# Performance work log

Hardware: AMD Instinct MI355X
Metric: run time of the kernel (lower is better)

## Reference

```python
import jax, jax.numpy as jnp
import numpy as np

B, N, F_RAW = 4, 131072, 9
GX, GY = 512, 512
EMB = 16
D_IN = F_RAW + EMB  # 25
D_OUT = 64
MAX_PT = 64
EPS = 1e-5


def _bn(x, g, b, w):
    # masked batch-statistics BatchNorm1d (training-mode forward); w: [P] 0/1 mask
    wc = w[:, None]
    cnt = jnp.maximum(w.sum(), 1.0)
    mu = (x * wc).sum(0) / cnt
    var = (((x - mu) ** 2) * wc).sum(0) / cnt
    return (x - mu) * jax.lax.rsqrt(var + EPS) * g + b


def setup_inputs() -> dict:
    key = jax.random.key(0)
    ks = jax.random.split(key, 12)
    pt_fea = jax.random.normal(ks[0], (B, N, F_RAW), jnp.float32)
    xy_ind = jax.random.randint(ks[1], (B, N, 2), 0, GX)
    pt_label = jax.random.randint(ks[2], (B, N, 1), 0, 32)

    def lin_w(k, i, o):
        return (jax.random.normal(k, (i, o), jnp.float32) / np.float32(np.sqrt(i)))

    return {
        "pt_fea": pt_fea, "xy_ind": xy_ind, "pt_label": pt_label,
        "emb": jax.random.normal(ks[3], (32, EMB), jnp.float32),
        "bn0_g": jnp.ones((D_IN,), jnp.float32), "bn0_b": jnp.zeros((D_IN,), jnp.float32),
        "w1": lin_w(ks[4], D_IN, 32), "b1": jnp.zeros((32,), jnp.float32),
        "bn1_g": jnp.ones((32,), jnp.float32), "bn1_b": jnp.zeros((32,), jnp.float32),
        "w2": lin_w(ks[5], 32, 64), "b2": jnp.zeros((64,), jnp.float32),
        "bn2_g": jnp.ones((64,), jnp.float32), "bn2_b": jnp.zeros((64,), jnp.float32),
        "w3": lin_w(ks[6], 64, D_OUT), "b3": jnp.zeros((D_OUT,), jnp.float32),
    }


def reference(pt_fea, xy_ind, pt_label, emb, bn0_g, bn0_b, w1, b1, bn1_g, bn1_b,
              w2, b2, bn2_g, bn2_b, w3, b3):
    P = B * N
    fea = pt_fea.reshape(P, F_RAW)
    ind = xy_ind.reshape(P, 2)
    batch_idx = jnp.repeat(jnp.arange(P // N), N)
    vox = (batch_idx * GX + ind[:, 0]) * GY + ind[:, 1]  # linearized (b, x, y)
    S = B * GX * GY

    # rank of each point within its voxel group (identity permutation; no shuffle)
    order = jnp.argsort(vox)  # stable
    sv = vox[order]
    pos = jnp.arange(P)
    is_new = jnp.concatenate([jnp.ones((1,), bool), sv[1:] != sv[:-1]])
    start = jax.lax.cummax(jnp.where(is_new, pos, 0))
    rank = jnp.zeros((P,), jnp.int32).at[order].set((pos - start).astype(jnp.int32))
    remain = rank < MAX_PT  # keep at most MAX_PT points per voxel
    mask = remain.astype(fea.dtype)

    x = jnp.concatenate([fea, emb[pt_label.reshape(P)]], axis=-1)  # [P, 25]
    x = _bn(x, bn0_g, bn0_b, mask)
    x = jax.nn.relu(_bn(x @ w1 + b1, bn1_g, bn1_b, mask))
    x = jax.nn.relu(_bn(x @ w2 + b2, bn2_g, bn2_b, mask))
    x = x @ w3 + b3  # [P, 64]

    # scatter_max over voxel groups; dropped points go to dummy segment S
    seg = jnp.where(remain, vox, S)
    pooled = jax.ops.segment_max(x, seg, num_segments=S + 1)[:S]
    cnt = jax.ops.segment_sum(mask, seg, num_segments=S + 1)[:S]
    pooled = jnp.where(cnt[:, None] > 0, pooled, 0.0)  # empty voxels stay 0

    bev = pooled.reshape(B, GX, GY, D_OUT).transpose(0, 3, 1, 2)  # [B, C, GX, GY]
    out = jax.lax.reduce_window(bev, -jnp.inf, jax.lax.max,
                                (1, 1, 3, 3), (1, 1, 1, 1),
                                [(0, 0), (0, 0), (1, 1), (1, 1)])
    return out
```

## Files before the change

### kernel.cpp

```cpp
#include <hip/hip_runtime.h>
#include <hip/hip_bf16.h>
#include <math.h>

typedef unsigned int u32;
typedef unsigned short u16;
typedef __attribute__((ext_vector_type(8))) short bf8v;
typedef __attribute__((ext_vector_type(4))) float f4v;

#define B_    4
#define N_    131072
#define P_    (B_*N_)
#define GX_   512
#define GY_   512
#define S_    (B_*GX_*GY_)
#define D_IN  25
#define MAXPT 64
#define EPS_  1e-5f
#define REP_  32

__device__ __forceinline__ float bf2f(u16 h){ return __uint_as_float(((u32)h)<<16); }
__device__ __forceinline__ u16 f2bf(float f){ u32 b=__float_as_uint(f); u32 r=b+0x7FFFu+((b>>16)&1u); return (u16)(r>>16); }

__device__ __forceinline__ void unpack8(uint4 a, float* x){
  x[0]=bf2f((u16)(a.x&0xFFFFu)); x[1]=bf2f((u16)(a.x>>16));
  x[2]=bf2f((u16)(a.y&0xFFFFu)); x[3]=bf2f((u16)(a.y>>16));
  x[4]=bf2f((u16)(a.z&0xFFFFu)); x[5]=bf2f((u16)(a.z>>16));
  x[6]=bf2f((u16)(a.w&0xFFFFu)); x[7]=bf2f((u16)(a.w>>16));
}

__device__ __forceinline__ void buildFeat(int p, const float* __restrict__ fea,
    const int* __restrict__ lab, const float* __restrict__ emb, float* v)
{
  #pragma unroll
  for (int k=0;k<9;k++) v[k] = fea[p*9+k];
  int l = lab[p];
  const float4* er = (const float4*)(emb + l*16);
  float4 e0=er[0], e1=er[1], e2=er[2], e3=er[3];
  v[9]=e0.x; v[10]=e0.y; v[11]=e0.z; v[12]=e0.w;
  v[13]=e1.x; v[14]=e1.y; v[15]=e1.z; v[16]=e1.w;
  v[17]=e2.x; v[18]=e2.y; v[19]=e2.z; v[20]=e2.w;
  v[21]=e3.x; v[22]=e3.y; v[23]=e3.z; v[24]=e3.w;
  #pragma unroll
  for (int k=25;k<32;k++) v[k]=0.f;
}

__device__ __forceinline__ void stats32(float* tile, float* sS, float* sQ,
                                        const float v[32], int tid)
{
  #pragma unroll
  for (int k=0;k<32;k++) tile[tid*33+k] = v[k];
  __syncthreads();
  int c = tid & 31, g = tid >> 5;
  float s=0.f, q=0.f;
  #pragma unroll
  for (int r=0;r<32;r++){
    float x = tile[(g*32+r)*33 + c];
    s += x; q = fmaf(x,x,q);
  }
  atomicAdd(&sS[c], s); atomicAdd(&sQ[c], q);
  __syncthreads();
}

__global__ __launch_bounds__(256) void zeroK(u32* __restrict__ cnt, float* __restrict__ stats)
{
  int t = blockIdx.x*256 + threadIdx.x;
  ((uint4*)cnt)[t] = make_uint4(0,0,0,0);
  if (blockIdx.x == 0){
    #pragma unroll
    for (int k=0;k<8;k++)
      ((uint4*)stats)[threadIdx.x*8+k] = make_uint4(0,0,0,0);
  }
}

__global__ __launch_bounds__(256) void passA(
    const float* __restrict__ fea, const int* __restrict__ xy, const int* __restrict__ lab,
    const float* __restrict__ emb, u32* __restrict__ cnt, u32* __restrict__ voxflag,
    float* __restrict__ partA)
{
  __shared__ float tile[256*33];
  __shared__ float sS[32], sQ[32];
  int tid = threadIdx.x;
  if (tid < 32){ sS[tid]=0.f; sQ[tid]=0.f; }
  int p = blockIdx.x*256 + tid;
  int b = p >> 17;
  int ix = xy[2*p], iy = xy[2*p+1];
  u32 vox = ((u32)b<<18) + ((u32)ix<<9) + (u32)iy;
  u32 rank = atomicAdd(&cnt[vox], 1u);
  bool remain = rank < MAXPT;
  voxflag[p] = vox | (min(rank,63u)<<20) | (remain ? 0x80000000u : 0u);

  float v[32];
  buildFeat(p, fea, lab, emb, v);
  if (!remain){
    #pragma unroll
    for (int k=0;k<32;k++) v[k]=0.f;
  }
  __syncthreads();
  stats32(tile, sS, sQ, v, tid);
  int rep = blockIdx.x & (REP_-1);
  if (tid < 32) atomicAdd(&partA[rep*64+tid], sS[tid]);
  else if (tid < 64) atomicAdd(&partA[rep*64+tid], sQ[tid-32]);
}

__global__ __launch_bounds__(256) void scan1(const u32* __restrict__ cnt,
                                             u32* __restrict__ scanned, u32* __restrict__ blockSum)
{
  __shared__ u32 ts[256];
  int tid = threadIdx.x;
  size_t base = (size_t)blockIdx.x*1024 + tid*4;
  uint4 c4 = *(const uint4*)(cnt + base);
  u32 c0=min(c4.x,64u), c1=min(c4.y,64u), c2=min(c4.z,64u), c3=min(c4.w,64u);
  u32 tsum = c0+c1+c2+c3;
  ts[tid]=tsum; __syncthreads();
  for (int off=1; off<256; off<<=1){
    u32 v = (tid>=off)? ts[tid-off] : 0u; __syncthreads();
    ts[tid]+=v; __syncthreads();
  }
  u32 ex = ts[tid]-tsum;
  uint4 o; o.x=ex; o.y=ex+c0; o.z=ex+c0+c1; o.w=ex+c0+c1+c2;
  *(uint4*)(scanned+base)=o;
  if (tid==255) blockSum[blockIdx.x]=ts[255];
}

__global__ __launch_bounds__(256) void scan2p0(u32* __restrict__ bs, u32* __restrict__ cntW,
    const float* __restrict__ partA,
    const float* __restrict__ g0, const float* __restrict__ b0,
    const float* __restrict__ w1, const float* __restrict__ b1,
    float* __restrict__ W1T, float* __restrict__ c1f)
{
  __shared__ u32 ts[256];
  __shared__ float red[64];
  __shared__ float s0[32], t0[32];
  __shared__ float Wsh;
  int tid=threadIdx.x;
  uint4 c4 = *(uint4*)(bs + tid*4);
  u32 tsum=c4.x+c4.y+c4.z+c4.w;
  ts[tid]=tsum; __syncthreads();
  for (int off=1;off<256;off<<=1){ u32 v=(tid>=off)?ts[tid-off]:0u; __syncthreads(); ts[tid]+=v; __syncthreads(); }
  u32 ex=ts[tid]-tsum;
  uint4 o; o.x=ex; o.y=ex+c4.x; o.z=ex+c4.x+c4.y; o.w=ex+c4.x+c4.y+c4.z;
  *(uint4*)(bs+tid*4)=o;
  if (tid==255){ *cntW = ts[255]; Wsh = fmaxf((float)ts[255],1.f); }
  if (tid < 64){
    float acc=0.f;
    for (int r=0;r<REP_;r++) acc += partA[r*64+tid];
    red[tid]=acc;
  }
  __syncthreads();
  if (tid < D_IN){
    float W = Wsh;
    float mu = red[tid]/W;
    float var = fmaxf(red[32+tid]/W - mu*mu, 0.f);
    float s = g0[tid]*rsqrtf(var+EPS_);
    s0[tid]=s; t0[tid]=b0[tid]-mu*s;
  }
  __syncthreads();
  if (tid < 32){
    float acc = b1[tid];
    #pragma unroll
    for (int i=0;i<D_IN;i++) acc = fmaf(t0[i], w1[i*32+tid], acc);
    c1f[tid] = acc;
    for (int i=0;i<32;i++) W1T[tid*32+i] = (i<D_IN)? s0[i]*w1[i*32+tid] : 0.f;
  }
}

__global__ void p1k(const float* __restrict__ partB, const u32* __restrict__ cntW,
                    const float* __restrict__ g, const float* __restrict__ bb,
                    float* __restrict__ sOut, float* __restrict__ tOut)
{
  int tid = threadIdx.x;
  float s=0.f, q=0.f;
  for (int r=0;r<REP_;r++){ s += partB[r*64+tid]; q += partB[r*64+32+tid]; }
  float W = fmaxf((float)(*cntW),1.f);
  float mu = s/W, var = fmaxf(q/W-mu*mu,0.f);
  float sc = g[tid]*rsqrtf(var+EPS_);
  sOut[tid]=sc; tOut[tid]=bb[tid]-mu*sc;
}
__global__ void p2k(const float* __restrict__ partC, const u32* __restrict__ cntW,
                    const float* __restrict__ g, const float* __restrict__ bb,
                    float* __restrict__ sOut, float* __restrict__ tOut)
{
  __shared__ float red[128];
  int tid = threadIdx.x;
  float acc=0.f;
  for (int r=0;r<REP_;r++) acc += partC[r*128+tid];
  red[tid]=acc;
  __syncthreads();
  if (tid < 64){
    float W = fmaxf((float)(*cntW),1.f);
    float mu = red[tid]/W, var = fmaxf(red[64+tid]/W-mu*mu,0.f);
    float s = g[tid]*rsqrtf(var+EPS_);
    sOut[tid]=s; tOut[tid]=bb[tid]-mu*s;
  }
}

__global__ __launch_bounds__(256) void passB(
    const float* __restrict__ fea, const int* __restrict__ lab, const float* __restrict__ emb,
    const u32* __restrict__ voxflag,
    const float* __restrict__ W1T, const float* __restrict__ c1f,
    u16* __restrict__ y1, float* __restrict__ partB)
{
  __shared__ float tile[256*33];
  __shared__ float sS[32], sQ[32];
  int tid = threadIdx.x;
  if (tid < 32){ sS[tid]=0.f; sQ[tid]=0.f; }
  int p = blockIdx.x*256 + tid;
  float x[32];
  buildFeat(p, fea, lab, emb, x);
  bool flag = (voxflag[p]>>31) != 0;
  float a[32];
  u32 outp[16];
  #pragma unroll
  for (int cc=0; cc<16; cc++){
    int c0 = 2*cc;
    float a0=c1f[c0], a1=c1f[c0+1];
    #pragma unroll
    for (int i=0;i<32;i++){ a0=fmaf(x[i], W1T[c0*32+i], a0); a1=fmaf(x[i], W1T[(c0+1)*32+i], a1); }
    if(!flag){a0=0.f;a1=0.f;}
    a[c0]=a0; a[c0+1]=a1;
    outp[cc] = (u32)f2bf(a0) | ((u32)f2bf(a1)<<16);
  }
  uint4* dst = (uint4*)(y1 + (size_t)p*32);
  dst[0]=make_uint4(outp[0],outp[1],outp[2],outp[3]);
  dst[1]=make_uint4(outp[4],outp[5],outp[6],outp[7]);
  dst[2]=make_uint4(outp[8],outp[9],outp[10],outp[11]);
  dst[3]=make_uint4(outp[12],outp[13],outp[14],outp[15]);
  __syncthreads();
  stats32(tile, sS, sQ, a, tid);
  int rep = blockIdx.x & (REP_-1);
  if (tid < 32) atomicAdd(&partB[rep*64+tid], sS[tid]);
  else if (tid < 64) atomicAdd(&partB[rep*64+tid], sQ[tid-32]);
}

__global__ __launch_bounds__(256) void passCM(const u16* __restrict__ y1,
    const u32* __restrict__ voxflag,
    const float* __restrict__ s1, const float* __restrict__ t1,
    const float* __restrict__ w2, const float* __restrict__ b2,
    u16* __restrict__ y2, float* __restrict__ partC)
{
  __shared__ u16 zt4[4][16*72];
  __shared__ float s1s[32], t1s[32];
  __shared__ float sS[64], sQ[64];
  int tid = threadIdx.x;
  if (tid < 32){ s1s[tid]=s1[tid]; t1s[tid]=t1[tid]; }
  if (tid < 64){ sS[tid]=0.f; sQ[tid]=0.f; }
  __syncthreads();
  int wv = tid>>6, l = tid&63;
  int p0 = blockIdx.x*64 + wv*16;
  int m = l&15, kc = l>>4;
  u16* zt = zt4[wv];

  bf8v Bf[4];
  #pragma unroll
  for (int nt=0;nt<4;nt++){
    #pragma unroll
    for (int j=0;j<8;j++)
      Bf[nt][j] = (short)f2bf(w2[(kc*8+j)*64 + nt*16 + m]);
  }
  uint4 ra = *(const uint4*)(y1 + (size_t)(p0+m)*32 + kc*8);
  float xv[8]; unpack8(ra, xv);
  bf8v Af;
  #pragma unroll
  for (int j=0;j<8;j++){
    int ch = kc*8+j;
    Af[j] = (short)f2bf(fmaxf(fmaf(xv[j], s1s[ch], t1s[ch]), 0.f));
  }
  unsigned long long msk = __ballot((l<16) && ((voxflag[p0+l]>>31)!=0));

  f4v acc[4];
  #pragma unroll
  for (int nt=0;nt<4;nt++){
    float bb = b2[nt*16+m];
    acc[nt] = (f4v){bb,bb,bb,bb};
    acc[nt] = __builtin_amdgcn_mfma_f32_16x16x32_bf16(Af, Bf[nt], acc[nt], 0,0,0);
  }
  #pragma unroll
  for (int nt=0;nt<4;nt++){
    #pragma unroll
    for (int r=0;r<4;r++){
      int row = kc*4+r;
      u16 val = ((msk>>row)&1ull) ? f2bf(acc[nt][r]) : (u16)0;
      zt[row*72 + nt*16+m] = val;
    }
  }
  __syncthreads();
  {
    float s=0.f, q=0.f;
    #pragma unroll
    for (int mi=0;mi<16;mi++){ float v = bf2f(zt[mi*72 + l]); s+=v; q=fmaf(v,v,q); }
    atomicAdd(&sS[l], s); atomicAdd(&sQ[l], q);
  }
  {
    int mm = l>>2, q4 = l&3;
    const uint4* src = (const uint4*)(zt + mm*72 + q4*16);
    uint4 v0 = src[0], v1 = src[1];
    uint4* dy = (uint4*)(y2 + (size_t)(p0+mm)*64 + q4*16);
    dy[0]=v0; dy[1]=v1;
  }
  __syncthreads();
  int rep = blockIdx.x & (REP_-1);
  if (tid < 64) atomicAdd(&partC[rep*128+tid], sS[tid]);
  else if (tid < 128) atomicAdd(&partC[rep*128+tid], sQ[tid-64]);
}

__global__ __launch_bounds__(256) void zpassM(const u16* __restrict__ y2,
    const u32* __restrict__ voxflag, const u32* __restrict__ scanned, const u32* __restrict__ bsum,
    const float* __restrict__ s2, const float* __restrict__ t2,
    const float* __restrict__ w3, const float* __restrict__ b3, u16* __restrict__ z)
{
  __shared__ u16 zt4[4][16*72];
  __shared__ float s2s[64], t2s[64];
  int tid = threadIdx.x;
  if (tid < 64){ s2s[tid]=s2[tid]; t2s[tid]=t2[tid]; }
  __syncthreads();
  int wv = tid>>6, l = tid&63;
  int p0 = blockIdx.x*64 + wv*16;
  int m = l&15, kc = l>>4;
  u16* zt = zt4[wv];

  bf8v Bf[4][2];
  #pragma unroll
  for (int nt=0;nt<4;nt++){
    #pragma unroll
    for (int kt=0;kt<2;kt++){
      #pragma unroll
      for (int j=0;j<8;j++)
        Bf[nt][kt][j] = (short)f2bf(w3[(kc*8+j+32*kt)*64 + nt*16 + m]);
    }
  }
  uint4 r0 = *(const uint4*)(y2 + (size_t)(p0+m)*64 + kc*8);
  uint4 r1 = *(const uint4*)(y2 + (size_t)(p0+m)*64 + 32 + kc*8);
  float x0[8], x1[8]; unpack8(r0,x0); unpack8(r1,x1);
  bf8v A0, A1;
  #pragma unroll
  for (int j=0;j<8;j++){
    int c0 = kc*8+j, c1 = 32+kc*8+j;
    A0[j] = (short)f2bf(fmaxf(fmaf(x0[j], s2s[c0], t2s[c0]), 0.f));
    A1[j] = (short)f2bf(fmaxf(fmaf(x1[j], s2s[c1], t2s[c1]), 0.f));
  }
  f4v acc[4];
  #pragma unroll
  for (int nt=0;nt<4;nt++){
    float bb = b3[nt*16+m];
    acc[nt] = (f4v){bb,bb,bb,bb};
    acc[nt] = __builtin_amdgcn_mfma_f32_16x16x32_bf16(A0, Bf[nt][0], acc[nt], 0,0,0);
    acc[nt] = __builtin_amdgcn_mfma_f32_16x16x32_bf16(A1, Bf[nt][1], acc[nt], 0,0,0);
  }
  #pragma unroll
  for (int nt=0;nt<4;nt++){
    #pragma unroll
    for (int r=0;r<4;r++)
      zt[(kc*4+r)*72 + nt*16+m] = f2bf(acc[nt][r]);
  }
  __syncthreads();
  int mm = l>>2, q4 = l&3;
  u32 vf = voxflag[p0+mm];
  if (vf>>31){
    u32 vox = vf & 0xFFFFFu;
    u32 rank = (vf>>20)&63u;
    u32 slot = scanned[vox] + bsum[vox>>10] + rank;
    const uint4* src = (const uint4*)(zt + mm*72 + q4*16);
    uint4 v0 = src[0], v1 = src[1];
    uint4* dz = (uint4*)(z + (size_t)slot*64 + q4*16);
    dz[0]=v0; dz[1]=v1;
  }
}

__global__ __launch_bounds__(256) void poolT(
    const u32* __restrict__ scanned, const u32* __restrict__ bsum, const u32* __restrict__ cnt,
    const u16* __restrict__ z, u16* __restrict__ pooledT)
{
  __shared__ u16 lds[32][66];
  int tid = threadIdx.x;
  int g = tid>>3, sub = tid&7;
  int v = blockIdx.x*32 + g;
  u32 n = min(cnt[v],64u);
  u16 r[8];
  if (n==0){
    #pragma unroll
    for (int j=0;j<8;j++) r[j]=0;
  } else {
    u32 st = scanned[v] + bsum[v>>10];
    float m[8];
    #pragma unroll
    for (int j=0;j<8;j++) m[j] = -__builtin_inff();
    for (u32 k=0;k<n;k++){
      uint4 a = *(const uint4*)(z + (size_t)(st+k)*64 + sub*8);
      float x[8]; unpack8(a,x);
      #pragma unroll
      for (int j=0;j<8;j++) m[j]=fmaxf(m[j],x[j]);
    }
    #pragma unroll
    for (int j=0;j<8;j++) r[j]=f2bf(m[j]);
  }
  #pragma unroll
  for (int j=0;j<8;j++) lds[g][sub*8+j] = r[j];
  __syncthreads();
  int c = tid>>2, q = tid&3;
  int v0 = blockIdx.x*32;
  int iy0 = v0 & 511, ix = (v0>>9)&511, b = v0>>18;
  u16 o[8];
  #pragma unroll
  for (int m2=0;m2<8;m2++) o[m2] = lds[q*8+m2][c];
  u16* dst = pooledT + (((size_t)(b*64+c)*512 + ix)*512 + iy0 + q*8);
  *(uint4*)dst = *(uint4*)o;
}

#define ITILE 32
__global__ __launch_bounds__(256) void dilate(const u16* __restrict__ pooledT, float* __restrict__ out)
{
  __shared__ float sh[2][516];
  int it = blockIdx.x;
  int c  = blockIdx.y;
  int b  = blockIdx.z;
  int tid = threadIdx.x;
  int j0 = tid*2;
  const u16* plane = pooledT + ((size_t)(b*64+c)*512)*512;
  float* oplane = out + ((size_t)(b*64+c)*512)*512;
  const float NINF = -__builtin_inff();
  if (tid==0){ sh[0][0]=NINF; sh[1][0]=NINF; }
  if (tid==255){ sh[0][513]=NINF; sh[1][513]=NINF; }
  int i0 = it*ITILE;

  float a0x,a0y,a1x,a1y,a2x,a2y;
  {
    int r = i0-1;
    if (r<0){ a0x=NINF; a0y=NINF; }
    else { u32 w=*(const u32*)(plane+(size_t)r*512+j0); a0x=bf2f((u16)(w&0xFFFFu)); a0y=bf2f((u16)(w>>16)); }
  }
  {
    u32 w=*(const u32*)(plane+(size_t)i0*512+j0); a1x=bf2f((u16)(w&0xFFFFu)); a1y=bf2f((u16)(w>>16));
  }
  for (int i=i0; i<i0+ITILE; i++){
    int r = i+1;
    if (r>511){ a2x=NINF; a2y=NINF; }
    else { u32 w=*(const u32*)(plane+(size_t)r*512+j0); a2x=bf2f((u16)(w&0xFFFFu)); a2y=bf2f((u16)(w>>16)); }
    int buf = i&1;
    sh[buf][1+j0] = fmaxf(fmaxf(a0x,a1x),a2x);
    sh[buf][2+j0] = fmaxf(fmaxf(a0y,a1y),a2y);
    __syncthreads();
    float s0=sh[buf][j0], s1=sh[buf][j0+1], s2=sh[buf][j0+2], s3=sh[buf][j0+3];
    float2 o = make_float2(fmaxf(fmaxf(s0,s1),s2), fmaxf(fmaxf(s1,s2),s3));
    *(float2*)(oplane + (size_t)i*512 + j0) = o;
    a0x=a1x; a0y=a1y; a1x=a2x; a1y=a2y;
  }
}

extern "C" void kernel_launch(void* const* d_in, const int* in_sizes, int n_in,
                              void* d_out, int out_size, void* d_ws, size_t ws_size,
                              hipStream_t stream) {
  const float* fea  = (const float*)d_in[0];
  const int*   xy   = (const int*)d_in[1];
  const int*   lab  = (const int*)d_in[2];
  const float* emb  = (const float*)d_in[3];
  const float* bn0g = (const float*)d_in[4];
  const float* bn0b = (const float*)d_in[5];
  const float* w1   = (const float*)d_in[6];
  const float* b1   = (const float*)d_in[7];
  const float* bn1g = (const float*)d_in[8];
  const float* bn1b = (const float*)d_in[9];
  const float* w2   = (const float*)d_in[10];
  const float* b2   = (const float*)d_in[11];
  const float* bn2g = (const float*)d_in[12];
  const float* bn2b = (const float*)d_in[13];
  const float* w3   = (const float*)d_in[14];
  const float* b3   = (const float*)d_in[15];

  char* ws = (char*)d_ws;
  size_t off = 0;
  u16*  z       = (u16*)(ws + off); off += (size_t)P_*64*2;
  u16*  pooledT = (u16*)(ws + off); off += (size_t)S_*64*2;
  u32*  cnt     = (u32*)(ws + off); off += (size_t)S_*4;
  u32*  scanned = (u32*)(ws + off); off += (size_t)S_*4;
  u32*  voxflag = (u32*)(ws + off); off += (size_t)P_*4;
  u32*  blockSum= (u32*)(ws + off); off += 4096;
  float* stats  = (float*)(ws + off);
  float* partA = stats + 0;
  float* partB = stats + 2048;
  float* partC = stats + 4096;
  u32*  cntW = (u32*)(stats + 8192);
  float* c1f = stats + 8256;
  float* s1  = stats + 8288;
  float* t1  = stats + 8320;
  float* s2  = stats + 8352;
  float* t2  = stats + 8416;
  float* W1T = stats + 8480;

  u16* y1 = (u16*)d_out;
  u16* y2 = (u16*)((char*)d_out + (size_t)P_*32*2);
  float* out = (float*)d_out;

  zeroK<<<S_/1024, 256, 0, stream>>>(cnt, stats);
  passA<<<P_/256, 256, 0, stream>>>(fea, xy, lab, emb, cnt, voxflag, partA);
  scan1<<<S_/1024, 256, 0, stream>>>(cnt, scanned, blockSum);
  scan2p0<<<1, 256, 0, stream>>>(blockSum, cntW, partA, bn0g, bn0b, w1, b1, W1T, c1f);
  passB<<<P_/256, 256, 0, stream>>>(fea, lab, emb, voxflag, W1T, c1f, y1, partB);
  p1k<<<1, 32, 0, stream>>>(partB, cntW, bn1g, bn1b, s1, t1);
  passCM<<<P_/64, 256, 0, stream>>>(y1, voxflag, s1, t1, w2, b2, y2, partC);
  p2k<<<1, 128, 0, stream>>>(partC, cntW, bn2g, bn2b, s2, t2);
  zpassM<<<P_/64, 256, 0, stream>>>(y2, voxflag, scanned, blockSum, s2, t2, w3, b3, z);
  poolT<<<S_/32, 256, 0, stream>>>(scanned, blockSum, cnt, z, pooledT);
  dim3 dg(GX_/ITILE, 64, B_);
  dilate<<<dg, 256, 0, stream>>>(pooledT, out);
}
```

Baseline: 336.5 us.

## Fuse final linear layer with voxel max-pooling via sorted point index

Adds a scatter kernel that builds a voxel-sorted point index, then replaces the separate z-projection and pooling kernels with one kernel. Each block owns 128 voxels, gathers its points' y2 rows, runs the last MFMA linear layer, and reduces into an LDS max buffer with order-preserving encoded atomicMax. This removes the full P×64 z intermediate write and re-read. In exchange it adds gathered y2 reads, LDS atomics, an extra launch, and per-tile syncs. Blocks also become imbalanced because each covers a variable number of points.

After: 358.7 us. 1.07x slower.

```diff
diff --git a/kernel.cpp b/kernel.cpp
--- a/kernel.cpp
+++ b/kernel.cpp
@@ -20,6 +20,8 @@
 
 __device__ __forceinline__ float bf2f(u16 h){ return __uint_as_float(((u32)h)<<16); }
 __device__ __forceinline__ u16 f2bf(float f){ u32 b=__float_as_uint(f); u32 r=b+0x7FFFu+((b>>16)&1u); return (u16)(r>>16); }
+__device__ __forceinline__ u32 encf(float f){ u32 b=__float_as_uint(f); return (b&0x80000000u)? ~b : (b|0x80000000u); }
+__device__ __forceinline__ float decf(u32 e){ return __uint_as_float((e&0x80000000u)? (e&0x7FFFFFFFu) : ~e); }
 
 __device__ __forceinline__ void unpack8(uint4 a, float* x){
   x[0]=bf2f((u16)(a.x&0xFFFFu)); x[1]=bf2f((u16)(a.x>>16));
@@ -164,6 +166,18 @@
   }
 }
 
+__global__ __launch_bounds__(256) void scatterK(const u32* __restrict__ voxflag,
+    const u32* __restrict__ scanned, const u32* __restrict__ bsum, u32* __restrict__ sortedIdx)
+{
+  int p = blockIdx.x*256+threadIdx.x;
+  u32 vf = voxflag[p];
+  if (vf>>31){
+    u32 vox = vf & 0xFFFFFu;
+    u32 rank = (vf>>20)&63u;
+    sortedIdx[scanned[vox] + bsum[vox>>10] + rank] = (u32)p;
+  }
+}
+
 __global__ void p1k(const float* __restrict__ partB, const u32* __restrict__ cntW,
                     const float* __restrict__ g, const float* __restrict__ bb,
                     float* __restrict__ sOut, float* __restrict__ tOut)
@@ -303,20 +317,28 @@
   else if (tid < 128) atomicAdd(&partC[rep*128+tid], sQ[tid-64]);
 }
 
-__global__ __launch_bounds__(256) void zpassM(const u16* __restrict__ y2,
-    const u32* __restrict__ voxflag, const u32* __restrict__ scanned, const u32* __restrict__ bsum,
+#define PVOX 128
+__global__ __launch_bounds__(256) void zpoolM(
+    const u32* __restrict__ sortedIdx, const u32* __restrict__ scanned,
+    const u32* __restrict__ bsum, const u32* __restrict__ cntW,
+    const u16* __restrict__ y2, const u32* __restrict__ voxflag,
     const float* __restrict__ s2, const float* __restrict__ t2,
-    const float* __restrict__ w3, const float* __restrict__ b3, u16* __restrict__ z)
-{
+    const float* __restrict__ w3, const float* __restrict__ b3,
+    u16* __restrict__ pooledT)
+{
+  __shared__ u32 pm[PVOX*66];
   __shared__ u16 zt4[4][16*72];
+  __shared__ unsigned char vl[64];
   __shared__ float s2s[64], t2s[64];
   int tid = threadIdx.x;
+  int v0 = blockIdx.x*PVOX;
   if (tid < 64){ s2s[tid]=s2[tid]; t2s[tid]=t2[tid]; }
-  __syncthreads();
+  for (int k=tid;k<PVOX*66;k+=256) pm[k]=0u;
+  u32 sBeg = scanned[v0] + bsum[v0>>10];
+  int vend = v0 + PVOX;
+  u32 sEnd = (vend == S_) ? *cntW : (scanned[vend] + bsum[vend>>10]);
   int wv = tid>>6, l = tid&63;
-  int p0 = blockIdx.x*64 + wv*16;
   int m = l&15, kc = l>>4;
-  u16* zt = zt4[wv];
 
   bf8v Bf[4][2];
   #pragma unroll
@@ -328,82 +350,74 @@
         Bf[nt][kt][j] = (short)f2bf(w3[(kc*8+j+32*kt)*64 + nt*16 + m]);
     }
   }
-  uint4 r0 = *(const uint4*)(y2 + (size_t)(p0+m)*64 + kc*8);
-  uint4 r1 = *(const uint4*)(y2 + (size_t)(p0+m)*64 + 32 + kc*8);
-  float x0[8], x1[8]; unpack8(r0,x0); unpack8(r1,x1);
-  bf8v A0, A1;
-  #pragma unroll
-  for (int j=0;j<8;j++){
-    int c0 = kc*8+j, c1 = 32+kc*8+j;
-    A0[j] = (short)f2bf(fmaxf(fmaf(x0[j], s2s[c0], t2s[c0]), 0.f));
-    A1[j] = (short)f2bf(fmaxf(fmaf(x1[j], s2s[c1], t2s[c1]), 0.f));
-  }
-  f4v acc[4];
-  #pragma unroll
-  for (int nt=0;nt<4;nt++){
-    float bb = b3[nt*16+m];
-    acc[nt] = (f4v){bb,bb,bb,bb};
-    acc[nt] = __builtin_amdgcn_mfma_f32_16x16x32_bf16(A0, Bf[nt][0], acc[nt], 0,0,0);
-    acc[nt] = __builtin_amdgcn_mfma_f32_16x16x32_bf16(A1, Bf[nt][1], acc[nt], 0,0,0);
-  }
-  #pragma unroll
-  for (int nt=0;nt<4;nt++){
-    #pragma unroll
-    for (int r=0;r<4;r++)
-      zt[(kc*4+r)*72 + nt*16+m] = f2bf(acc[nt][r]);
-  }
-  __syncthreads();
-  int mm = l>>2, q4 = l&3;
-  u32 vf = voxflag[p0+mm];
-  if (vf>>31){
-    u32 vox = vf & 0xFFFFFu;
-    u32 rank = (vf>>20)&63u;
-    u32 slot = scanned[vox] + bsum[vox>>10] + rank;
-    const uint4* src = (const uint4*)(zt + mm*72 + q4*16);
-    uint4 v0 = src[0], v1 = src[1];
-    uint4* dz = (uint4*)(z + (size_t)slot*64 + q4*16);
-    dz[0]=v0; dz[1]=v1;
-  }
-}
-
-__global__ __launch_bounds__(256) void poolT(
-    const u32* __restrict__ scanned, const u32* __restrict__ bsum, const u32* __restrict__ cnt,
-    const u16* __restrict__ z, u16* __restrict__ pooledT)
-{
-  __shared__ u16 lds[32][66];
-  int tid = threadIdx.x;
-  int g = tid>>3, sub = tid&7;
-  int v = blockIdx.x*32 + g;
-  u32 n = min(cnt[v],64u);
-  u16 r[8];
-  if (n==0){
-    #pragma unroll
-    for (int j=0;j<8;j++) r[j]=0;
-  } else {
-    u32 st = scanned[v] + bsum[v>>10];
-    float m[8];
-    #pragma unroll
-    for (int j=0;j<8;j++) m[j] = -__builtin_inff();
-    for (u32 k=0;k<n;k++){
-      uint4 a = *(const uint4*)(z + (size_t)(st+k)*64 + sub*8);
-      float x[8]; unpack8(a,x);
+  __syncthreads();
+
+  int ntile = (int)((sEnd - sBeg + 63u)>>6);
+  for (int t5=0; t5<ntile; ++t5){
+    u32 slot = sBeg + (u32)t5*64u + (u32)(wv*16+m);
+    bool valid = slot < sEnd;
+    u32 p = valid ? sortedIdx[slot] : 0u;
+    if (kc==0)
+      vl[wv*16+m] = valid ? (unsigned char)((voxflag[p]&0xFFFFFu) - (u32)v0) : (unsigned char)255;
+    uint4 r0 = *(const uint4*)(y2 + (size_t)p*64 + kc*8);
+    uint4 r1 = *(const uint4*)(y2 + (size_t)p*64 + 32 + kc*8);
+    float x0[8], x1[8]; unpack8(r0,x0); unpack8(r1,x1);
+    bf8v A0, A1;
+    #pragma unroll
+    for (int j=0;j<8;j++){
+      int c0 = kc*8+j, c1 = 32+kc*8+j;
+      A0[j] = (short)f2bf(fmaxf(fmaf(x0[j], s2s[c0], t2s[c0]), 0.f));
+      A1[j] = (short)f2bf(fmaxf(fmaf(x1[j], s2s[c1], t2s[c1]), 0.f));
+    }
+    f4v acc[4];
+    #pragma unroll
+    for (int nt=0;nt<4;nt++){
+      float bb = b3[nt*16+m];
+      acc[nt] = (f4v){bb,bb,bb,bb};
+      acc[nt] = __builtin_amdgcn_mfma_f32_16x16x32_bf16(A0, Bf[nt][0], acc[nt], 0,0,0);
+      acc[nt] = __builtin_amdgcn_mfma_f32_16x16x32_bf16(A1, Bf[nt][1], acc[nt], 0,0,0);
+    }
+    u16* zt = zt4[wv];
+    #pragma unroll
+    for (int nt=0;nt<4;nt++){
       #pragma unroll
-      for (int j=0;j<8;j++) m[j]=fmaxf(m[j],x[j]);
-    }
-    #pragma unroll
-    for (int j=0;j<8;j++) r[j]=f2bf(m[j]);
-  }
-  #pragma unroll
-  for (int j=0;j<8;j++) lds[g][sub*8+j] = r[j];
-  __syncthreads();
-  int c = tid>>2, q = tid&3;
-  int v0 = blockIdx.x*32;
-  int iy0 = v0 & 511, ix = (v0>>9)&511, b = v0>>18;
-  u16 o[8];
-  #pragma unroll
-  for (int m2=0;m2<8;m2++) o[m2] = lds[q*8+m2][c];
-  u16* dst = pooledT + (((size_t)(b*64+c)*512 + ix)*512 + iy0 + q*8);
-  *(uint4*)dst = *(uint4*)o;
+      for (int r=0;r<4;r++)
+        zt[(kc*4+r)*72 + nt*16+m] = f2bf(acc[nt][r]);
+    }
+    __syncthreads();
+    {
+      int c = tid & 63, rg = tid>>6;
+      float mx = 0.f; int curv = -1;
+      for (int rr=rg*16; rr<rg*16+16; ++rr){
+        int vv = vl[rr];
+        if (vv==255) continue;
+        float zz = bf2f(zt4[rr>>4][(rr&15)*72 + c]);
+        if (vv != curv){
+          if (curv>=0) atomicMax(&pm[curv*66+c], encf(mx));
+          curv = vv; mx = zz;
+        } else {
+          mx = fmaxf(mx, zz);
+        }
+      }
+      if (curv>=0) atomicMax(&pm[curv*66+c], encf(mx));
+    }
+    __syncthreads();
+  }
+
+  {
+    int c = tid&63, seg = tid>>6;
+    int iy0 = (v0 & 511) + seg*32;
+    int ix = (v0>>9)&511, b = v0>>18;
+    u16 ob[32];
+    #pragma unroll
+    for (int j=0;j<32;j++){
+      u32 e = pm[(seg*32+j)*66 + c];
+      ob[j] = (e==0u) ? (u16)0 : f2bf(decf(e));
+    }
+    u16* dst = pooledT + (((size_t)(b*64+c)*512 + ix)*512 + iy0);
+    #pragma unroll
+    for (int q=0;q<4;q++) ((uint4*)dst)[q] = ((uint4*)ob)[q];
+  }
 }
 
 #define ITILE 32
@@ -468,11 +482,11 @@
 
   char* ws = (char*)d_ws;
   size_t off = 0;
-  u16*  z       = (u16*)(ws + off); off += (size_t)P_*64*2;
   u16*  pooledT = (u16*)(ws + off); off += (size_t)S_*64*2;
   u32*  cnt     = (u32*)(ws + off); off += (size_t)S_*4;
   u32*  scanned = (u32*)(ws + off); off += (size_t)S_*4;
   u32*  voxflag = (u32*)(ws + off); off += (size_t)P_*4;
+  u32*  sortedIdx=(u32*)(ws + off); off += (size_t)P_*4;
   u32*  blockSum= (u32*)(ws + off); off += 4096;
   float* stats  = (float*)(ws + off);
   float* partA = stats + 0;
@@ -494,12 +508,13 @@
   passA<<<P_/256, 256, 0, stream>>>(fea, xy, lab, emb, cnt, voxflag, partA);
   scan1<<<S_/1024, 256, 0, stream>>>(cnt, scanned, blockSum);
   scan2p0<<<1, 256, 0, stream>>>(blockSum, cntW, partA, bn0g, bn0b, w1, b1, W1T, c1f);
+  scatterK<<<P_/256, 256, 0, stream>>>(voxflag, scanned, blockSum, sortedIdx);
   passB<<<P_/256, 256, 0, stream>>>(fea, lab, emb, voxflag, W1T, c1f, y1, partB);
   p1k<<<1, 32, 0, stream>>>(partB, cntW, bn1g, bn1b, s1, t1);
   passCM<<<P_/64, 256, 0, stream>>>(y1, voxflag, s1, t1, w2, b2, y2, partC);
   p2k<<<1, 128, 0, stream>>>(partC, cntW, bn2g, bn2b, s2, t2);
-  zpassM<<<P_/64, 256, 0, stream>>>(y2, voxflag, scanned, blockSum, s2, t2, w3, b3, z);
-  poolT<<<S_/32, 256, 0, stream>>>(scanned, blockSum, cnt, z, pooledT);
+  zpoolM<<<S_/PVOX, 256, 0, stream>>>(sortedIdx, scanned, blockSum, cntW,
+                                      y2, voxflag, s2, t2, w3, b3, pooledT);
   dim3 dg(GX_/ITILE, 64, B_);
   dilate<<<dg, 256, 0, stream>>>(pooledT, out);
 }
```
